# Kernel tuning notes

Measured on AMD Instinct MI355X. Metric: run time of the kernel, lower is better.

The kernel has to match this reference:

```python
import jax, jax.numpy as jnp
import numpy as np

G, S, M = 4, 2048, 1024   # groups (batch), tokens per group, emb dim
E, H, K = 8, 4096, 2      # experts, mlp dim, top-k
CAP = int(K * S / E * 1.25)  # expert capacity = 640
AUX_COEF, Z_COEF = 0.01, 0.001


def setup_inputs() -> dict:
    key = jax.random.key(0)
    k1, k2, k3, k4, k5 = jax.random.split(key, 5)
    return {
        "inputs": jax.random.normal(k1, (G, S, M), jnp.float32),
        "paddings": jnp.zeros((G, S), jnp.float32),  # 1.0 = padded token
        "router_w": jax.random.normal(k2, (M, E), jnp.float32) / np.sqrt(M),
        "wi_gate": jax.random.normal(k3, (E, M, H), jnp.float32) / np.sqrt(M),
        "wi_0": jax.random.normal(k4, (E, M, H), jnp.float32) / np.sqrt(M),
        "wo": jax.random.normal(k5, (E, H, M), jnp.float32) / np.sqrt(H),
    }


def reference(inputs, paddings, router_w, wi_gate, wi_0, wo):
    # Router
    logits = jnp.einsum('gsm,me->gse', inputs, router_w)          # [G,S,E]
    probs = jax.nn.softmax(logits, axis=-1)
    top_p, top_i = jax.lax.top_k(probs, K)                        # [G,S,K]

    nonpad = 1.0 - paddings                                       # [G,S]
    exp_mask = jax.nn.one_hot(top_i, E, dtype=jnp.float32)        # [G,S,K,E]
    exp_mask = exp_mask * nonpad[:, :, None, None]

    # Position in expert (capacity-limited), priority by token order then k slot
    mask_flat = exp_mask.reshape(G, S * K, E)
    pos = jnp.cumsum(mask_flat, axis=1) * mask_flat               # 1-indexed where assigned
    keep = mask_flat * (pos <= CAP)
    pos_oh = jax.nn.one_hot((pos - 1.0).astype(jnp.int32), CAP, dtype=jnp.float32)  # [G,SK,E,CAP]
    dispatch_k = (keep[..., None] * pos_oh).reshape(G, S, K, E, CAP)
    dispatch = dispatch_k.sum(axis=2)                             # [G,S,E,CAP]
    combine = jnp.einsum('gsk,gskec->gsec', top_p, dispatch_k)    # [G,S,E,CAP]

    # Dispatch -> gated expert FFN -> combine
    expert_in = jnp.einsum('gsec,gsm->egcm', dispatch, inputs)    # [E,G,CAP,M]
    h = jax.nn.silu(jnp.einsum('egcm,emh->egch', expert_in, wi_gate)) \
        * jnp.einsum('egcm,emh->egch', expert_in, wi_0)           # [E,G,CAP,H]
    expert_out = jnp.einsum('egch,ehm->egcm', h, wo)              # [E,G,CAP,M]
    output = jnp.einsum('gsec,egcm->gsm', combine, expert_out)    # [G,S,M]

    # Aux losses: load-balancing (Switch style) + router z-loss
    em = jnp.max(jax.nn.one_hot(top_i, E, dtype=jnp.float32), axis=-2)       # [G,S,E]
    lb = jnp.mean(jnp.mean(em, axis=-2) * jnp.mean(probs, axis=-2)) * E * E
    z = jnp.mean(jax.nn.logsumexp(logits, axis=-1) ** 2)
    aux_loss = AUX_COEF * lb + Z_COEF * z
    return output, aux_loss
```

## Files before the change

### kernel.cpp

```cpp
#include <hip/hip_runtime.h>
#include <hip/hip_bf16.h>
#include <math.h>

#define G 4
#define S 2048
#define MDIM 1024
#define E 8
#define HDIM 4096
#define TOPK 2
#define CAP 640
#define GC (G*CAP)

typedef __attribute__((ext_vector_type(8))) short bf16x8;
typedef __attribute__((ext_vector_type(4))) short s16x4;
typedef __attribute__((ext_vector_type(4))) float f32x4;
typedef unsigned int u32;
typedef unsigned short u16;

#define MFMA16(a,b,c) __builtin_amdgcn_mfma_f32_16x16x32_bf16(a,b,c,0,0,0)
#define SB0() __builtin_amdgcn_sched_barrier(0)
#define BAR() __builtin_amdgcn_s_barrier()
#define LGKM0() asm volatile("s_waitcnt lgkmcnt(0)" ::: "memory")

__device__ __forceinline__ u16 f2bf(float f) {
    union { float f; u32 u; } v; v.f = f;
    u32 r = v.u + 0x7fffu + ((v.u >> 16) & 1u);
    return (u16)(r >> 16);
}

__device__ __forceinline__ void gload16(const char* gp, char* lp) {
    __builtin_amdgcn_global_load_lds((const __attribute__((address_space(1))) u32*)gp,
                                     (__attribute__((address_space(3))) u32*)lp,
                                     16, 0, 0);
}

__device__ __forceinline__ int swzb(int r) { return ((r >> 1) & 3) << 4; }

__global__ __launch_bounds__(256) void transpose_cvt(const float* __restrict__ in,
                                                     u16* __restrict__ out, int R, int C) {
    int e = blockIdx.z;
    const float* ine = in + (size_t)e * R * C;
    u16* oute = out + (size_t)e * R * C;
    __shared__ float tile[64][68];
    int t = threadIdx.x;
    int x0 = blockIdx.x * 64, y0 = blockIdx.y * 64;
    int lx = (t & 15) * 4, ly = t >> 4;
    #pragma unroll
    for (int i = 0; i < 4; ++i) {
        f32x4 v = *(const f32x4*)(ine + (size_t)(y0 + ly + i * 16) * C + x0 + lx);
        *(f32x4*)&tile[ly + i * 16][lx] = v;
    }
    __syncthreads();
    int rr0 = (t & 15) * 4, cb = t >> 4;
    #pragma unroll
    for (int p = 0; p < 4; ++p) {
        int cc = cb + p * 16;
        s16x4 pk;
        #pragma unroll
        for (int j = 0; j < 4; ++j) pk[j] = (short)f2bf(tile[rr0 + j][cc]);
        *(s16x4*)(oute + (size_t)(x0 + cc) * R + y0 + rr0) = pk;
    }
}

__global__ __launch_bounds__(256) void router_kernel(const float* __restrict__ inp,
                                                     const float* __restrict__ rw,
                                                     int* __restrict__ top_i,
                                                     float* __restrict__ top_p,
                                                     float* __restrict__ partials) {
    int wid = threadIdx.x >> 6, lane = threadIdx.x & 63;
    int tok = blockIdx.x * 4 + wid;
    const float* x = inp + (size_t)tok * MDIM;
    float acc[E] = {0.f,0.f,0.f,0.f,0.f,0.f,0.f,0.f};
    #pragma unroll
    for (int rep = 0; rep < 4; ++rep) {
        int m0 = rep * 256 + lane * 4;
        f32x4 xv = *(const f32x4*)(x + m0);
        #pragma unroll
        for (int j = 0; j < 4; ++j) {
            const float* r = rw + (size_t)(m0 + j) * E;
            float xj = xv[j];
            #pragma unroll
            for (int e = 0; e < E; ++e) acc[e] += xj * r[e];
        }
    }
    #pragma unroll
    for (int e = 0; e < E; ++e)
        #pragma unroll
        for (int off = 32; off; off >>= 1) acc[e] += __shfl_down(acc[e], off);

    __shared__ float part[4][17];
    if (lane == 0) {
        float mx = acc[0];
        #pragma unroll
        for (int e = 1; e < E; ++e) mx = fmaxf(mx, acc[e]);
        float p[E], sum = 0.f;
        #pragma unroll
        for (int e = 0; e < E; ++e) { p[e] = expf(acc[e] - mx); sum += p[e]; }
        float inv = 1.f / sum;
        #pragma unroll
        for (int e = 0; e < E; ++e) p[e] *= inv;
        float lse = logf(sum) + mx;
        int i0 = 0;
        #pragma unroll
        for (int e = 1; e < E; ++e) if (acc[e] > acc[i0]) i0 = e;
        int i1 = (i0 == 0) ? 1 : 0;
        #pragma unroll
        for (int e = 0; e < E; ++e) if (e != i0 && acc[e] > acc[i1]) i1 = e;
        top_i[tok*2+0] = i0; top_i[tok*2+1] = i1;
        top_p[tok*2+0] = p[i0]; top_p[tok*2+1] = p[i1];
        #pragma unroll
        for (int e = 0; e < E; ++e) { part[wid][e] = p[e]; part[wid][8+e] = 0.f; }
        part[wid][8+i0] = 1.f; part[wid][8+i1] = 1.f;
        part[wid][16] = lse * lse;
    }
    __syncthreads();
    if (threadIdx.x < 17) {
        float v = part[0][threadIdx.x] + part[1][threadIdx.x] +
                  part[2][threadIdx.x] + part[3][threadIdx.x];
        partials[(size_t)blockIdx.x * 17 + threadIdx.x] = v;
    }
}

__global__ __launch_bounds__(256) void reduce_partials(const float* __restrict__ partials,
                                                       float* __restrict__ sums) {
    int g = blockIdx.x, t = threadIdx.x;
    float loc[17];
    #pragma unroll
    for (int c = 0; c < 17; ++c) loc[c] = 0.f;
    for (int r = t; r < 1024; r += 256) {
        const float* pr = partials + ((size_t)g * 1024 + r) * 17;
        #pragma unroll
        for (int c = 0; c < 17; ++c) loc[c] += pr[c];
    }
    __shared__ float red[256];
    for (int c = 0; c < 17; ++c) {
        red[t] = loc[c]; __syncthreads();
        for (int off = 128; off; off >>= 1) {
            if (t < off) red[t] += red[t + off];
            __syncthreads();
        }
        if (t == 0) sums[g * 17 + c] = red[0];
        __syncthreads();
    }
}

__global__ void aux_final(const float* __restrict__ sums, float* __restrict__ out) {
    float lb = 0.f, z = 0.f;
    for (int g = 0; g < G; ++g) {
        for (int e = 0; e < E; ++e)
            lb += (sums[g*17 + 8 + e] / (float)S) * (sums[g*17 + e] / (float)S);
        z += sums[g*17 + 16];
    }
    lb = lb / (float)(G * E) * (float)(E * E);
    z /= (float)(G * S);
    out[(size_t)G * S * MDIM] = 0.01f * lb + 0.001f * z;
}

__global__ __launch_bounds__(256) void scan_kernel(const int* __restrict__ top_i,
                                                   const float* __restrict__ pad,
                                                   int* __restrict__ slot_token,
                                                   int* __restrict__ token_c) {
    int b = blockIdx.x; int g = b >> 3, e = b & 7;
    int t = threadIdx.x;
    __shared__ int sums[256];
    int base = t * 16;
    int run = 0; unsigned mask16 = 0; int loc[16];
    #pragma unroll
    for (int j = 0; j < 16; ++j) {
        int i = base + j; int s = i >> 1, k = i & 1;
        int ex = top_i[((size_t)(g * S + s)) * 2 + k];
        int m = (ex == e) && (pad[g * S + s] == 0.f);
        run += m; loc[j] = run; mask16 |= ((unsigned)m << j);
    }
    sums[t] = run; __syncthreads();
    for (int off = 1; off < 256; off <<= 1) {
        int v = (t >= off) ? sums[t - off] : 0;
        __syncthreads();
        sums[t] += v;
        __syncthreads();
    }
    int excl = sums[t] - run;
    #pragma unroll
    for (int j = 0; j < 16; ++j) {
        if ((mask16 >> j) & 1u) {
            int pos = excl + loc[j];
            if (pos <= CAP) {
                int i = base + j; int s = i >> 1, k = i & 1;
                slot_token[((size_t)(e * G + g)) * CAP + (pos - 1)] = s;
                token_c[((size_t)(g * S + s)) * 2 + k] = pos - 1;
            }
        }
    }
}

__global__ __launch_bounds__(128) void gather_kernel(const float* __restrict__ inp,
                                                     const int* __restrict__ slot_token,
                                                     u16* __restrict__ X) {
    int row = blockIdx.x;
    int t = threadIdx.x;
    int s = slot_token[row];
    int g = (row % GC) / CAP;
    bf16x8 v;
    if (s >= 0) {
        const float* src = inp + ((size_t)(g * S + s)) * MDIM + t * 8;
        f32x4 a = *(const f32x4*)src;
        f32x4 b = *(const f32x4*)(src + 4);
        #pragma unroll
        for (int j = 0; j < 4; ++j) { v[j] = (short)f2bf(a[j]); v[4+j] = (short)f2bf(b[j]); }
    } else {
        #pragma unroll
        for (int j = 0; j < 8; ++j) v[j] = 0;
    }
    *(bf16x8*)(X + (size_t)row * MDIM + t * 8) = v;
}

__global__ __launch_bounds__(512, 1) void gemm_ffn12_v7(
        const u16* __restrict__ Xb, const u16* __restrict__ WgT,
        const u16* __restrict__ W0T, u16* __restrict__ Hb) {
    extern __shared__ char smem[];
    const int NK = MDIM / 32;
    int bid = blockIdx.x;
    int swz = (bid & 7) * 320 + (bid >> 3);
    int mt = swz % 10, nt = (swz / 10) & 31, e = swz / 320;
    const char* A  = (const char*)(Xb  + (size_t)e * GC * MDIM   + (size_t)mt * 256 * MDIM);
    const char* Bg = (const char*)(WgT + (size_t)e * HDIM * MDIM + (size_t)nt * 128 * MDIM);
    const char* B0 = (const char*)(W0T + (size_t)e * HDIM * MDIM + (size_t)nt * 128 * MDIM);
    int tid = threadIdx.x, w = tid >> 6, l = tid & 63;
    int wm = w >> 2, wn = w & 3;
    int rl = l >> 2, cch = (l & 3) * 16;
    int fr = l & 15, fg = l >> 4;
    int lswz = ((fr >> 1) & 3) << 4;

    int rA0 = (0 * 8 + w) * 16 + rl, rA1 = (1 * 8 + w) * 16 + rl, rB = w * 16 + rl;
    const char* gA0 = A  + (size_t)rA0 * MDIM * 2 + (cch ^ swzb(rA0));
    const char* gA1 = A  + (size_t)rA1 * MDIM * 2 + (cch ^ swzb(rA1));
    const char* gBg = Bg + (size_t)rB  * MDIM * 2 + (cch ^ swzb(rB));
    const char* gB0 = B0 + (size_t)rB  * MDIM * 2 + (cch ^ swzb(rB));
    int baseA = (wm * 128 + fr) * 64 + ((fg * 16) ^ lswz);
    int baseB = (wn * 32  + fr) * 64 + ((fg * 16) ^ lswz);

    f32x4 ag[8][2], ao[8][2];
    #pragma unroll
    for (int i = 0; i < 8; ++i) {
        ag[i][0] = (f32x4){0,0,0,0}; ag[i][1] = (f32x4){0,0,0,0};
        ao[i][0] = (f32x4){0,0,0,0}; ao[i][1] = (f32x4){0,0,0,0};
    }

    auto stage = [&](int tt) {
        int kk = tt * 64, b = tt & 3;
        gload16(gA0 + kk, smem + b * 16384 + (0 * 8 + w) * 1024);
        gload16(gA1 + kk, smem + b * 16384 + (1 * 8 + w) * 1024);
        gload16(gBg + kk, smem + 65536 + b * 8192 + w * 1024);
        gload16(gB0 + kk, smem + 98304 + b * 8192 + w * 1024);
    };

    stage(0); stage(1);
    asm volatile("s_waitcnt vmcnt(4)" ::: "memory");
    BAR();

    #pragma unroll 1
    for (int t = 0; t < NK; ++t) {
        if (t + 2 < NK) stage(t + 2);
        const char* bufA = smem + (t & 3) * 16384 + baseA;
        const char* pG = smem + 65536 + (t & 3) * 8192 + baseB;
        const char* pO = smem + 98304 + (t & 3) * 8192 + baseB;
        bf16x8 bgf[2], bof[2], af[4];
        bgf[0] = *(const bf16x8*)(pG);  bgf[1] = *(const bf16x8*)(pG + 1024);
        bof[0] = *(const bf16x8*)(pO);  bof[1] = *(const bf16x8*)(pO + 1024);
        #pragma unroll
        for (int i = 0; i < 4; ++i) af[i] = *(const bf16x8*)(bufA + i * 1024);
        SB0();
        BAR();
        LGKM0(); SB0();
        __builtin_amdgcn_s_setprio(1);
        #pragma unroll
        for (int fm = 0; fm < 4; ++fm)
            #pragma unroll
            for (int fn = 0; fn < 2; ++fn) {
                ag[fm][fn] = MFMA16(bgf[fn], af[fm], ag[fm][fn]);
                ao[fm][fn] = MFMA16(bof[fn], af[fm], ao[fm][fn]);
            }
        __builtin_amdgcn_s_setprio(0);
        BAR();
        bf16x8 ah[4];
        #pragma unroll
        for (int i = 0; i < 4; ++i) ah[i] = *(const bf16x8*)(bufA + (4 + i) * 1024);
        SB0();
        if (t + 2 < NK) { asm volatile("s_waitcnt vmcnt(4)" ::: "memory"); }
        else            { asm volatile("s_waitcnt vmcnt(0)" ::: "memory"); }
        BAR();
        LGKM0(); SB0();
        __builtin_amdgcn_s_setprio(1);
        #pragma unroll
        for (int fm = 0; fm < 4; ++fm)
            #pragma unroll
            for (int fn = 0; fn < 2; ++fn) {
                ag[4+fm][fn] = MFMA16(bgf[fn], ah[fm], ag[4+fm][fn]);
                ao[4+fm][fn] = MFMA16(bof[fn], ah[fm], ao[4+fm][fn]);
            }
        __builtin_amdgcn_s_setprio(0);
        BAR();
    }

    u16* He = Hb + (size_t)e * GC * HDIM;
    int row0 = mt * 256 + wm * 128 + fr;
    int col0 = nt * 128 + wn * 32 + fg * 4;
    #pragma unroll
    for (int fm = 0; fm < 8; ++fm)
        #pragma unroll
        for (int fn = 0; fn < 2; ++fn) {
            s16x4 pk;
            #pragma unroll
            for (int r = 0; r < 4; ++r) {
                float gv = ag[fm][fn][r], ov = ao[fm][fn][r];
                float hv = gv / (1.f + __expf(-gv)) * ov;
                pk[r] = (short)f2bf(hv);
            }
            *(s16x4*)(He + (size_t)(row0 + fm * 16) * HDIM + col0 + fn * 16) = pk;
        }
}

__global__ __launch_bounds__(512, 1) void gemm_out_v7(
        const u16* __restrict__ Hb, const u16* __restrict__ WoT,
        float* __restrict__ EO) {
    extern __shared__ char smem[];
    const int NK = HDIM / 32;
    int bid = blockIdx.x;
    int swz = (bid & 7) * 80 + (bid >> 3);
    int nt = swz & 3, mt = (swz / 4) % 20, e = swz / 80;
    const char* A = (const char*)(Hb  + (size_t)e * GC * HDIM   + (size_t)mt * 128 * HDIM);
    const char* B = (const char*)(WoT + (size_t)e * MDIM * HDIM + (size_t)nt * 256 * HDIM);
    int tid = threadIdx.x, w = tid >> 6, l = tid & 63;
    int wm = w >> 2, wn = w & 3;
    int rl = l >> 2, cch = (l & 3) * 16;
    int fr = l & 15, fg = l >> 4;
    int lswz = ((fr >> 1) & 3) << 4;

    int rA = w * 16 + rl, rB0 = (0 * 8 + w) * 16 + rl, rB1 = (1 * 8 + w) * 16 + rl;
    const char* gA  = A + (size_t)rA  * HDIM * 2 + (cch ^ swzb(rA));
    const char* gBa = B + (size_t)rB0 * HDIM * 2 + (cch ^ swzb(rB0));
    const char* gBb = B + (size_t)rB1 * HDIM * 2 + (cch ^ swzb(rB1));
    int baseA = (wm * 64 + fr) * 64 + ((fg * 16) ^ lswz);
    int baseB = (wn * 64 + fr) * 64 + ((fg * 16) ^ lswz);

    f32x4 acc[4][4];
    #pragma unroll
    for (int i = 0; i < 4; ++i)
        #pragma unroll
        for (int j = 0; j < 4; ++j) acc[i][j] = (f32x4){0,0,0,0};

    auto stage = [&](int tt) {
        int kk = tt * 64, b = tt & 3;
        gload16(gA  + kk, smem + b * 8192 + w * 1024);
        gload16(gBa + kk, smem + 32768 + b * 16384 + (0 * 8 + w) * 1024);
        gload16(gBb + kk, smem + 32768 + b * 16384 + (1 * 8 + w) * 1024);
    };

    stage(0); stage(1);
    asm volatile("s_waitcnt vmcnt(3)" ::: "memory");
    BAR();

    #pragma unroll 1
    for (int t = 0; t < NK; ++t) {
        if (t + 2 < NK) stage(t + 2);
        const char* pA = smem + (t & 3) * 8192 + baseA;
        const char* pB = smem + 32768 + (t & 3) * 16384 + baseB;
        bf16x8 af[4], bf[4];
        #pragma unroll
        for (int i = 0; i < 4; ++i) {
            af[i] = *(const bf16x8*)(pA + i * 1024);
            bf[i] = *(const bf16x8*)(pB + i * 1024);
        }
        SB0();
        if (t + 2 < NK) { asm volatile("s_waitcnt vmcnt(3)" ::: "memory"); }
        else            { asm volatile("s_waitcnt vmcnt(0)" ::: "memory"); }
        BAR();
        LGKM0(); SB0();
        __builtin_amdgcn_s_setprio(1);
        #pragma unroll
        for (int fm = 0; fm < 4; ++fm)
            #pragma unroll
            for (int fn = 0; fn < 4; ++fn)
                acc[fm][fn] = MFMA16(bf[fn], af[fm], acc[fm][fn]);
        __builtin_amdgcn_s_setprio(0);
        BAR();
    }

    float* Ee = EO + (size_t)e * GC * MDIM;
    int row0 = mt * 128 + wm * 64 + fr;
    int col0 = nt * 256 + wn * 64 + fg * 4;
    #pragma unroll
    for (int fm = 0; fm < 4; ++fm)
        #pragma unroll
        for (int fn = 0; fn < 4; ++fn)
            *(f32x4*)(Ee + (size_t)(row0 + fm * 16) * MDIM + col0 + fn * 16) = acc[fm][fn];
}

__global__ __launch_bounds__(256) void combine_kernel(const float* __restrict__ EO,
                                                      const int* __restrict__ top_i,
                                                      const float* __restrict__ top_p,
                                                      const int* __restrict__ token_c,
                                                      float* __restrict__ out) {
    int tok = blockIdx.x, t = threadIdx.x;
    int g = tok >> 11;
    f32x4 acc = {0.f, 0.f, 0.f, 0.f};
    #pragma unroll
    for (int k = 0; k < 2; ++k) {
        int c = token_c[tok * 2 + k];
        if (c >= 0) {
            int e = top_i[tok * 2 + k];
            float p = top_p[tok * 2 + k];
            const float* src = EO + ((size_t)e * GC + g * CAP + c) * MDIM + t * 4;
            f32x4 v = *(const f32x4*)src;
            #pragma unroll
            for (int j = 0; j < 4; ++j) acc[j] += p * v[j];
        }
    }
    *(f32x4*)(out + (size_t)tok * MDIM + t * 4) = acc;
}

extern "C" void kernel_launch(void* const* d_in, const int* in_sizes, int n_in,
                              void* d_out, int out_size, void* d_ws, size_t ws_size,
                              hipStream_t stream) {
    (void)in_sizes; (void)n_in; (void)out_size; (void)ws_size;
    const float* inputs   = (const float*)d_in[0];
    const float* paddings = (const float*)d_in[1];
    const float* router_w = (const float*)d_in[2];
    const float* wi_gate  = (const float*)d_in[3];
    const float* wi_0     = (const float*)d_in[4];
    const float* wo       = (const float*)d_in[5];
    float* out = (float*)d_out;

    char* p = (char*)d_ws;
    u16* WgT = (u16*)p; p += (size_t)E * HDIM * MDIM * 2;
    u16* W0T = (u16*)p; p += (size_t)E * HDIM * MDIM * 2;
    u16* WoT = (u16*)p; p += (size_t)E * HDIM * MDIM * 2;
    u16* Xb  = (u16*)p; p += (size_t)E * GC * MDIM * 2;
    u16* Hb  = (u16*)p; p += (size_t)E * GC * HDIM * 2;
    float* EO = (float*)p; p += (size_t)E * GC * MDIM * 4;
    int*   top_i = (int*)p;   p += (size_t)G * S * TOPK * 4;
    float* top_p = (float*)p; p += (size_t)G * S * TOPK * 4;
    int*   token_c = (int*)p; p += (size_t)G * S * TOPK * 4;
    int*   slot_token = (int*)p; p += (size_t)E * G * CAP * 4;
    float* partials = (float*)p; p += (size_t)4096 * 17 * 4;
    float* sums = (float*)p; p += 4 * 17 * 4;

    hipMemsetAsync(token_c, 0xFF, (size_t)G * S * TOPK * 4, stream);
    hipMemsetAsync(slot_token, 0xFF, (size_t)E * G * CAP * 4, stream);

    hipFuncSetAttribute((const void*)gemm_ffn12_v7,
                        hipFuncAttributeMaxDynamicSharedMemorySize, 131072);
    hipFuncSetAttribute((const void*)gemm_out_v7,
                        hipFuncAttributeMaxDynamicSharedMemorySize, 98304);

    transpose_cvt<<<dim3(HDIM/64, MDIM/64, E), 256, 0, stream>>>(wi_gate, WgT, MDIM, HDIM);
    transpose_cvt<<<dim3(HDIM/64, MDIM/64, E), 256, 0, stream>>>(wi_0,   W0T, MDIM, HDIM);
    transpose_cvt<<<dim3(MDIM/64, HDIM/64, E), 256, 0, stream>>>(wo,     WoT, HDIM, MDIM);

    router_kernel<<<G * S / 4, 256, 0, stream>>>(inputs, router_w, top_i, top_p, partials);
    reduce_partials<<<G, 256, 0, stream>>>(partials, sums);
    scan_kernel<<<G * E, 256, 0, stream>>>(top_i, paddings, slot_token, token_c);
    gather_kernel<<<E * GC, 128, 0, stream>>>(inputs, slot_token, Xb);
    gemm_ffn12_v7<<<2560, 512, 131072, stream>>>(Xb, WgT, W0T, Hb);
    gemm_out_v7<<<640, 512, 98304, stream>>>(Hb, WoT, EO);
    combine_kernel<<<G * S, 256, 0, stream>>>(EO, top_i, top_p, token_c, out);
    aux_final<<<1, 1, 0, stream>>>(sums, out);
}
```

Baseline: 817.8 us.

## Load B operand fragments directly from global into registers, staging only A in LDS

Both expert GEMMs stop staging the weight (B) tiles through LDS. Each wave now loads its own B fragments straight from global memory into double-buffered registers one K-step ahead, and only the activation (A) tile keeps the LDS pipeline. This cuts LDS traffic, shared-memory allocation and per-iteration barriers, and removes the scheduling barriers. The trade-off is that B reads become uncoalesced 16-byte per-lane global loads that duplicate data across the waves sharing a column tile. It also adds register pressure and global-latency exposure.

```diff
diff --git a/kernel.cpp b/kernel.cpp
--- a/kernel.cpp
+++ b/kernel.cpp
@@ -18,9 +18,7 @@
 typedef unsigned short u16;
 
 #define MFMA16(a,b,c) __builtin_amdgcn_mfma_f32_16x16x32_bf16(a,b,c,0,0,0)
-#define SB0() __builtin_amdgcn_sched_barrier(0)
 #define BAR() __builtin_amdgcn_s_barrier()
-#define LGKM0() asm volatile("s_waitcnt lgkmcnt(0)" ::: "memory")
 
 __device__ __forceinline__ u16 f2bf(float f) {
     union { float f; u32 u; } v; v.f = f;
@@ -214,7 +212,7 @@
     *(bf16x8*)(X + (size_t)row * MDIM + t * 8) = v;
 }
 
-__global__ __launch_bounds__(512, 1) void gemm_ffn12_v7(
+__global__ __launch_bounds__(512, 1) void gemm_ffn12_v8(
         const u16* __restrict__ Xb, const u16* __restrict__ WgT,
         const u16* __restrict__ W0T, u16* __restrict__ Hb) {
     extern __shared__ char smem[];
@@ -231,13 +229,15 @@
     int fr = l & 15, fg = l >> 4;
     int lswz = ((fr >> 1) & 3) << 4;
 
-    int rA0 = (0 * 8 + w) * 16 + rl, rA1 = (1 * 8 + w) * 16 + rl, rB = w * 16 + rl;
-    const char* gA0 = A  + (size_t)rA0 * MDIM * 2 + (cch ^ swzb(rA0));
-    const char* gA1 = A  + (size_t)rA1 * MDIM * 2 + (cch ^ swzb(rA1));
-    const char* gBg = Bg + (size_t)rB  * MDIM * 2 + (cch ^ swzb(rB));
-    const char* gB0 = B0 + (size_t)rB  * MDIM * 2 + (cch ^ swzb(rB));
+    int rA0 = (0 * 8 + w) * 16 + rl, rA1 = (1 * 8 + w) * 16 + rl;
+    const char* gA0 = A + (size_t)rA0 * MDIM * 2 + (cch ^ swzb(rA0));
+    const char* gA1 = A + (size_t)rA1 * MDIM * 2 + (cch ^ swzb(rA1));
     int baseA = (wm * 128 + fr) * 64 + ((fg * 16) ^ lswz);
-    int baseB = (wn * 32  + fr) * 64 + ((fg * 16) ^ lswz);
+
+    const char* pBg0 = Bg + (size_t)(wn * 32 + 0 * 16 + fr) * MDIM * 2 + fg * 16;
+    const char* pBg1 = Bg + (size_t)(wn * 32 + 1 * 16 + fr) * MDIM * 2 + fg * 16;
+    const char* pBo0 = B0 + (size_t)(wn * 32 + 0 * 16 + fr) * MDIM * 2 + fg * 16;
+    const char* pBo1 = B0 + (size_t)(wn * 32 + 1 * 16 + fr) * MDIM * 2 + fg * 16;
 
     f32x4 ag[8][2], ao[8][2];
     #pragma unroll
@@ -250,56 +250,47 @@
         int kk = tt * 64, b = tt & 3;
         gload16(gA0 + kk, smem + b * 16384 + (0 * 8 + w) * 1024);
         gload16(gA1 + kk, smem + b * 16384 + (1 * 8 + w) * 1024);
-        gload16(gBg + kk, smem + 65536 + b * 8192 + w * 1024);
-        gload16(gB0 + kk, smem + 98304 + b * 8192 + w * 1024);
     };
 
+    bf16x8 bgA[2], boA[2], bgB[2], boB[2];
+
     stage(0); stage(1);
-    asm volatile("s_waitcnt vmcnt(4)" ::: "memory");
+    bgA[0] = *(const bf16x8*)(pBg0);  bgA[1] = *(const bf16x8*)(pBg1);
+    boA[0] = *(const bf16x8*)(pBo0);  boA[1] = *(const bf16x8*)(pBo1);
+    asm volatile("s_waitcnt vmcnt(6)" ::: "memory");
     BAR();
 
-    #pragma unroll 1
-    for (int t = 0; t < NK; ++t) {
+    auto body = [&](int t, bf16x8 (&bgc)[2], bf16x8 (&boc)[2],
+                    bf16x8 (&bgn)[2], bf16x8 (&bon)[2]) {
+        const char* bufA = smem + (t & 3) * 16384 + baseA;
+        bf16x8 af[8];
+        #pragma unroll
+        for (int i = 0; i < 8; ++i) af[i] = *(const bf16x8*)(bufA + i * 1024);
+        if (t + 1 < NK) {
+            int kk = (t + 1) * 64;
+            bgn[0] = *(const bf16x8*)(pBg0 + kk);  bgn[1] = *(const bf16x8*)(pBg1 + kk);
+            bon[0] = *(const bf16x8*)(pBo0 + kk);  bon[1] = *(const bf16x8*)(pBo1 + kk);
+        }
         if (t + 2 < NK) stage(t + 2);
-        const char* bufA = smem + (t & 3) * 16384 + baseA;
-        const char* pG = smem + 65536 + (t & 3) * 8192 + baseB;
-        const char* pO = smem + 98304 + (t & 3) * 8192 + baseB;
-        bf16x8 bgf[2], bof[2], af[4];
-        bgf[0] = *(const bf16x8*)(pG);  bgf[1] = *(const bf16x8*)(pG + 1024);
-        bof[0] = *(const bf16x8*)(pO);  bof[1] = *(const bf16x8*)(pO + 1024);
-        #pragma unroll
-        for (int i = 0; i < 4; ++i) af[i] = *(const bf16x8*)(bufA + i * 1024);
-        SB0();
+        if (t + 2 < NK)      { asm volatile("s_waitcnt vmcnt(6)" ::: "memory"); }
+        else if (t + 1 < NK) { asm volatile("s_waitcnt vmcnt(4)" ::: "memory"); }
+        else                 { asm volatile("s_waitcnt vmcnt(0)" ::: "memory"); }
         BAR();
-        LGKM0(); SB0();
         __builtin_amdgcn_s_setprio(1);
         #pragma unroll
-        for (int fm = 0; fm < 4; ++fm)
+        for (int fm = 0; fm < 8; ++fm)
             #pragma unroll
             for (int fn = 0; fn < 2; ++fn) {
-                ag[fm][fn] = MFMA16(bgf[fn], af[fm], ag[fm][fn]);
-                ao[fm][fn] = MFMA16(bof[fn], af[fm], ao[fm][fn]);
+                ag[fm][fn] = MFMA16(bgc[fn], af[fm], ag[fm][fn]);
+                ao[fm][fn] = MFMA16(boc[fn], af[fm], ao[fm][fn]);
             }
         __builtin_amdgcn_s_setprio(0);
-        BAR();
-        bf16x8 ah[4];
-        #pragma unroll
-        for (int i = 0; i < 4; ++i) ah[i] = *(const bf16x8*)(bufA + (4 + i) * 1024);
-        SB0();
-        if (t + 2 < NK) { asm volatile("s_waitcnt vmcnt(4)" ::: "memory"); }
-        else            { asm volatile("s_waitcnt vmcnt(0)" ::: "memory"); }
-        BAR();
-        LGKM0(); SB0();
-        __builtin_amdgcn_s_setprio(1);
-        #pragma unroll
-        for (int fm = 0; fm < 4; ++fm)
-            #pragma unroll
-            for (int fn = 0; fn < 2; ++fn) {
-                ag[4+fm][fn] = MFMA16(bgf[fn], ah[fm], ag[4+fm][fn]);
-                ao[4+fm][fn] = MFMA16(bof[fn], ah[fm], ao[4+fm][fn]);
-            }
-        __builtin_amdgcn_s_setprio(0);
-        BAR();
+    };
+
+    #pragma unroll 1
+    for (int t = 0; t < NK; t += 2) {
+        body(t, bgA, boA, bgB, boB);
+        body(t + 1, bgB, boB, bgA, boA);
     }
 
     u16* He = Hb + (size_t)e * GC * HDIM;
@@ -320,7 +311,7 @@
         }
 }
 
-__global__ __launch_bounds__(512, 1) void gemm_out_v7(
+__global__ __launch_bounds__(512, 1) void gemm_out_v8(
         const u16* __restrict__ Hb, const u16* __restrict__ WoT,
         float* __restrict__ EO) {
     extern __shared__ char smem[];
@@ -336,12 +327,14 @@
     int fr = l & 15, fg = l >> 4;
     int lswz = ((fr >> 1) & 3) << 4;
 
-    int rA = w * 16 + rl, rB0 = (0 * 8 + w) * 16 + rl, rB1 = (1 * 8 + w) * 16 + rl;
-    const char* gA  = A + (size_t)rA  * HDIM * 2 + (cch ^ swzb(rA));
-    const char* gBa = B + (size_t)rB0 * HDIM * 2 + (cch ^ swzb(rB0));
-    const char* gBb = B + (size_t)rB1 * HDIM * 2 + (cch ^ swzb(rB1));
+    int rA = w * 16 + rl;
+    const char* gA = A + (size_t)rA * HDIM * 2 + (cch ^ swzb(rA));
     int baseA = (wm * 64 + fr) * 64 + ((fg * 16) ^ lswz);
-    int baseB = (wn * 64 + fr) * 64 + ((fg * 16) ^ lswz);
+
+    const char* pB0 = B + (size_t)(wn * 64 + 0 * 16 + fr) * HDIM * 2 + fg * 16;
+    const char* pB1 = B + (size_t)(wn * 64 + 1 * 16 + fr) * HDIM * 2 + fg * 16;
+    const char* pB2 = B + (size_t)(wn * 64 + 2 * 16 + fr) * HDIM * 2 + fg * 16;
+    const char* pB3 = B + (size_t)(wn * 64 + 3 * 16 + fr) * HDIM * 2 + fg * 16;
 
     f32x4 acc[4][4];
     #pragma unroll
@@ -351,39 +344,45 @@
 
     auto stage = [&](int tt) {
         int kk = tt * 64, b = tt & 3;
-        gload16(gA  + kk, smem + b * 8192 + w * 1024);
-        gload16(gBa + kk, smem + 32768 + b * 16384 + (0 * 8 + w) * 1024);
-        gload16(gBb + kk, smem + 32768 + b * 16384 + (1 * 8 + w) * 1024);
+        gload16(gA + kk, smem + b * 8192 + w * 1024);
     };
 
+    bf16x8 bA[4], bB[4];
+
     stage(0); stage(1);
-    asm volatile("s_waitcnt vmcnt(3)" ::: "memory");
+    bA[0] = *(const bf16x8*)(pB0);  bA[1] = *(const bf16x8*)(pB1);
+    bA[2] = *(const bf16x8*)(pB2);  bA[3] = *(const bf16x8*)(pB3);
+    asm volatile("s_waitcnt vmcnt(5)" ::: "memory");
     BAR();
 
-    #pragma unroll 1
-    for (int t = 0; t < NK; ++t) {
+    auto body = [&](int t, bf16x8 (&bc)[4], bf16x8 (&bn)[4]) {
+        const char* pA = smem + (t & 3) * 8192 + baseA;
+        bf16x8 af[4];
+        #pragma unroll
+        for (int i = 0; i < 4; ++i) af[i] = *(const bf16x8*)(pA + i * 1024);
+        if (t + 1 < NK) {
+            int kk = (t + 1) * 64;
+            bn[0] = *(const bf16x8*)(pB0 + kk);  bn[1] = *(const bf16x8*)(pB1 + kk);
+            bn[2] = *(const bf16x8*)(pB2 + kk);  bn[3] = *(const bf16x8*)(pB3 + kk);
+        }
         if (t + 2 < NK) stage(t + 2);
-        const char* pA = smem + (t & 3) * 8192 + baseA;
-        const char* pB = smem + 32768 + (t & 3) * 16384 + baseB;
-        bf16x8 af[4], bf[4];
-        #pragma unroll
-        for (int i = 0; i < 4; ++i) {
-            af[i] = *(const bf16x8*)(pA + i * 1024);
-            bf[i] = *(const bf16x8*)(pB + i * 1024);
-        }
-        SB0();
-        if (t + 2 < NK) { asm volatile("s_waitcnt vmcnt(3)" ::: "memory"); }
-        else            { asm volatile("s_waitcnt vmcnt(0)" ::: "memory"); }
+        if (t + 2 < NK)      { asm volatile("s_waitcnt vmcnt(5)" ::: "memory"); }
+        else if (t + 1 < NK) { asm volatile("s_waitcnt vmcnt(4)" ::: "memory"); }
+        else                 { asm volatile("s_waitcnt vmcnt(0)" ::: "memory"); }
         BAR();
-        LGKM0(); SB0();
         __builtin_amdgcn_s_setprio(1);
         #pragma unroll
         for (int fm = 0; fm < 4; ++fm)
             #pragma unroll
             for (int fn = 0; fn < 4; ++fn)
-                acc[fm][fn] = MFMA16(bf[fn], af[fm], acc[fm][fn]);
+                acc[fm][fn] = MFMA16(bc[fn], af[fm], acc[fm][fn]);
         __builtin_amdgcn_s_setprio(0);
-        BAR();
+    };
+
+    #pragma unroll 1
+    for (int t = 0; t < NK; t += 2) {
+        body(t, bA, bB);
+        body(t + 1, bB, bA);
     }
 
     float* Ee = EO + (size_t)e * GC * MDIM;
@@ -448,10 +447,10 @@
     hipMemsetAsync(token_c, 0xFF, (size_t)G * S * TOPK * 4, stream);
     hipMemsetAsync(slot_token, 0xFF, (size_t)E * G * CAP * 4, stream);
 
-    hipFuncSetAttribute((const void*)gemm_ffn12_v7,
-                        hipFuncAttributeMaxDynamicSharedMemorySize, 131072);
-    hipFuncSetAttribute((const void*)gemm_out_v7,
-                        hipFuncAttributeMaxDynamicSharedMemorySize, 98304);
+    hipFuncSetAttribute((const void*)gemm_ffn12_v8,
+                        hipFuncAttributeMaxDynamicSharedMemorySize, 65536);
+    hipFuncSetAttribute((const void*)gemm_out_v8,
+                        hipFuncAttributeMaxDynamicSharedMemorySize, 32768);
 
     transpose_cvt<<<dim3(HDIM/64, MDIM/64, E), 256, 0, stream>>>(wi_gate, WgT, MDIM, HDIM);
     transpose_cvt<<<dim3(HDIM/64, MDIM/64, E), 256, 0, stream>>>(wi_0,   W0T, MDIM, HDIM);
@@ -461,8 +460,8 @@
     reduce_partials<<<G, 256, 0, stream>>>(partials, sums);
     scan_kernel<<<G * E, 256, 0, stream>>>(top_i, paddings, slot_token, token_c);
     gather_kernel<<<E * GC, 128, 0, stream>>>(inputs, slot_token, Xb);
-    gemm_ffn12_v7<<<2560, 512, 131072, stream>>>(Xb, WgT, W0T, Hb);
-    gemm_out_v7<<<640, 512, 98304, stream>>>(Hb, WoT, EO);
+    gemm_ffn12_v8<<<2560, 512, 65536, stream>>>(Xb, WgT, W0T, Hb);
+    gemm_out_v8<<<640, 512, 32768, stream>>>(Hb, WoT, EO);
     combine_kernel<<<G * S, 256, 0, stream>>>(EO, top_i, top_p, token_c, out);
     aux_final<<<1, 1, 0, stream>>>(sums, out);
 }
```

After: 1.057 ms. 29.3% more time.
